# Optimization experiments

Hardware: AMD Instinct MI355X
Metric: run time of the kernel (lower is better)

Reference implementation:

```python
import jax, jax.numpy as jnp
import numpy as np

N, D, H, K = 32768, 1024, 8, 2048
HD = D // H
SIM_THRESH = 0.9


def setup_inputs() -> dict:
    key = jax.random.key(0)
    ks = jax.random.split(key, 12)
    s = 1.0 / np.sqrt(D)
    return {
        "roi_features": jax.random.normal(ks[0], (N, D), jnp.float32),
        "w_score": jax.random.uniform(ks[1], (1, D), jnp.float32, -s, s),
        "b_score": jax.random.uniform(ks[2], (1,), jnp.float32, -s, s),
        "wq": jax.random.uniform(ks[3], (D, D), jnp.float32, -s, s),
        "bq": jax.random.uniform(ks[4], (D,), jnp.float32, -s, s),
        "wk": jax.random.uniform(ks[5], (D, D), jnp.float32, -s, s),
        "bk": jax.random.uniform(ks[6], (D,), jnp.float32, -s, s),
        "wv": jax.random.uniform(ks[7], (D, D), jnp.float32, -s, s),
        "bv": jax.random.uniform(ks[8], (D,), jnp.float32, -s, s),
        "wo": jax.random.uniform(ks[9], (D, 2 * D), jnp.float32, -s, s),
        "bo": jax.random.uniform(ks[10], (D,), jnp.float32, -s, s),
    }


def _cross_frame_attention(src, dst, wq, bq, wk, bk, wv, bv, wo, bo):
    # src, dst: [K, D] -> fused dst: [K, D]
    q = (dst @ wq.T + bq).reshape(-1, H, HD).transpose(1, 0, 2)  # [H,K,HD]
    k = (src @ wk.T + bk).reshape(-1, H, HD).transpose(1, 0, 2)
    v = (src @ wv.T + bv).reshape(-1, H, HD).transpose(1, 0, 2)
    logits = jnp.einsum("hqd,hkd->hqk", q, k) / np.sqrt(HD)
    qn = q / (jnp.linalg.norm(q, axis=-1, keepdims=True) + 1e-6)
    kn = k / (jnp.linalg.norm(k, axis=-1, keepdims=True) + 1e-6)
    sim = jnp.einsum("hqd,hkd->hqk", qn, kn)
    valid = sim > SIM_THRESH
    logits = jnp.where(valid, logits, -10000.0)
    attn = jax.nn.softmax(logits, axis=-1)
    has_match = jnp.any(valid, axis=-1, keepdims=True)
    attn = jnp.where(has_match, attn, 0.0)  # dropout is identity in eval
    agg = jnp.einsum("hqk,hkd->hqd", attn, v).transpose(1, 0, 2).reshape(dst.shape[0], D)
    return jnp.concatenate([agg, dst], axis=-1) @ wo.T + bo


def reference(roi_features, w_score, b_score, wq, bq, wk, bk, wv, bv, wo, bo):
    # _global_fusion_fallback path (no temporal context set)
    scores = (roi_features @ w_score.T + b_score)[:, 0]  # [N]
    _, topk_idx = jax.lax.top_k(scores, K)
    selected = roi_features[topk_idx]  # [K, D]
    fused = _cross_frame_attention(selected, selected, wq, bq, wk, bk, wv, bv, wo, bo)
    return roi_features.at[topk_idx].set(0.5 * selected + 0.5 * fused)
```

## Files before the change

### kernel.cpp

```cpp
#include <hip/hip_runtime.h>
#include <cstddef>

typedef unsigned int u32;
typedef unsigned short u16;
typedef short v8s __attribute__((ext_vector_type(8)));
typedef float v4f __attribute__((ext_vector_type(4)));

#define N_ROWS 32768
#define DIM 1024
#define NHEAD 8
#define HD 128
#define KSEL 2048

static __device__ __forceinline__ u16 f2bf(float f) {
  u32 u = __float_as_uint(f);
  u32 r = (u + 0x7FFFu + ((u >> 16) & 1u)) >> 16;
  return (u16)r;
}
static __device__ __forceinline__ float bf2f(u16 b) {
  return __uint_as_float(((u32)b) << 16);
}
static __device__ __forceinline__ u32 mono(float s) {
  u32 b = __float_as_uint(s);
  return (b & 0x80000000u) ? ~b : (b | 0x80000000u);
}

__global__ __launch_bounds__(256) void score_copy_kernel(
    const float* __restrict__ roi, const float* __restrict__ wsc,
    const float* __restrict__ bsc, float* __restrict__ out,
    float* __restrict__ scores) {
  const int w = threadIdx.x >> 6, lane = threadIdx.x & 63;
  const int row = blockIdx.x * 4 + w;
  const float4* r4 = (const float4*)(roi + (size_t)row * DIM);
  const float4* w4 = (const float4*)wsc;
  float4* o4 = (float4*)(out + (size_t)row * DIM);
  float sum = 0.f;
#pragma unroll
  for (int rep = 0; rep < 4; ++rep) {
    int i = rep * 64 + lane;
    float4 v = r4[i];
    float4 q = w4[i];
    sum += v.x * q.x + v.y * q.y + v.z * q.z + v.w * q.w;
    o4[i] = v;
  }
#pragma unroll
  for (int d = 1; d < 64; d <<= 1) sum += __shfl_xor(sum, d);
  if (lane == 0) scores[row] = sum + bsc[0];
}

__global__ __launch_bounds__(256) void cvt4_kernel(
    const float* __restrict__ wq, const float* __restrict__ wk,
    const float* __restrict__ wv, const float* __restrict__ wo,
    u16* __restrict__ wqb, u16* __restrict__ wkb,
    u16* __restrict__ wvb, u16* __restrict__ wob) {
  const int M = DIM * DIM;
  long long i = ((long long)blockIdx.x * 256 + threadIdx.x) * 4;
  const float* src;
  u16* dst;
  if (i < M) {
    src = wq; dst = wqb;
  } else if (i < 2LL * M) {
    src = wk; dst = wkb; i -= M;
  } else if (i < 3LL * M) {
    src = wv; dst = wvb; i -= 2LL * M;
  } else {
    src = wo; dst = wob; i -= 3LL * M;
  }
  float4 v = *(const float4*)(src + i);
  ushort4 o = make_ushort4(f2bf(v.x), f2bf(v.y), f2bf(v.z), f2bf(v.w));
  *(ushort4*)(dst + i) = o;
}

__global__ __launch_bounds__(1024) void topk_kernel(const float* __restrict__ scores,
                                                    int* __restrict__ out_idx) {
  __shared__ u32 hist[256];
  __shared__ int sneed;
  __shared__ u32 sprefix;
  __shared__ int scan_gt[1024];
  __shared__ int scan_eq[1024];
  const int tid = threadIdx.x;
  if (tid == 0) { sneed = KSEL; sprefix = 0u; }
  for (int pass = 0; pass < 4; ++pass) {
    const int shift = 24 - pass * 8;
    if (tid < 256) hist[tid] = 0u;
    __syncthreads();
    const u32 prefmask = (pass == 0) ? 0u : (0xFFFFFFFFu << (shift + 8));
    const u32 pref = sprefix;
    for (int i = tid; i < N_ROWS; i += 1024) {
      u32 key = mono(scores[i]);
      if ((key & prefmask) == pref) atomicAdd(&hist[(key >> shift) & 255u], 1u);
    }
    __syncthreads();
    if (tid == 0) {
      int need = sneed;
      u32 cum = 0;
      int b = 255;
      for (; b > 0; --b) {
        if (cum + hist[b] >= (u32)need) break;
        cum += hist[b];
      }
      sneed = need - (int)cum;
      sprefix = pref | ((u32)b << shift);
    }
    __syncthreads();
  }
  const u32 T = sprefix;
  const int base = tid * 32;
  int cgt = 0, ceq = 0;
  for (int j = 0; j < 32; ++j) {
    u32 key = mono(scores[base + j]);
    cgt += (key > T);
    ceq += (key == T);
  }
  scan_gt[tid] = cgt;
  scan_eq[tid] = ceq;
  __syncthreads();
  for (int off = 1; off < 1024; off <<= 1) {
    int a = (tid >= off) ? scan_gt[tid - off] : 0;
    int b = (tid >= off) ? scan_eq[tid - off] : 0;
    __syncthreads();
    scan_gt[tid] += a;
    scan_eq[tid] += b;
    __syncthreads();
  }
  const int gt_off = scan_gt[tid] - cgt;
  const int eq_off = scan_eq[tid] - ceq;
  const int total_gt = scan_gt[1023];
  int g = gt_off, e = eq_off;
  for (int j = 0; j < 32; ++j) {
    u32 key = mono(scores[base + j]);
    if (key > T) {
      out_idx[g++] = base + j;
    } else if (key == T) {
      if (total_gt + e < KSEL) out_idx[total_gt + e] = base + j;
      e++;
    }
  }
}

__global__ __launch_bounds__(256) void gather_kernel(const float* __restrict__ out,
                                                     const int* __restrict__ idx,
                                                     u16* __restrict__ xo) {
  const int j = blockIdx.x;
  const int row = idx[j];
  const int c = threadIdx.x * 4;
  float4 v = *(const float4*)(out + (size_t)row * DIM + c);
  ushort4 o = make_ushort4(f2bf(v.x), f2bf(v.y), f2bf(v.z), f2bf(v.w));
  *(ushort4*)(xo + (size_t)j * 2048 + 1024 + c) = o;
}

template <int OUT_MODE>
__global__ __launch_bounds__(256) void gemm_xwt_kernel(
    const u16* __restrict__ A, int lda, const u16* __restrict__ W, int ldw,
    const float* __restrict__ bias, void* __restrict__ Cout, int ldc, int Kd) {
  __shared__ __align__(16) u16 As[64][40];
  __shared__ __align__(16) u16 Bs[64][40];
  const int m0 = blockIdx.y * 64, n0 = blockIdx.x * 64;
  const int w = threadIdx.x >> 6, lane = threadIdx.x & 63;
  const int t = lane & 15, quad = lane >> 4;
  const int srow = threadIdx.x >> 2, skc = (threadIdx.x & 3) * 8;
  v4f acc[4];
#pragma unroll
  for (int i = 0; i < 4; ++i) acc[i] = (v4f){0.f, 0.f, 0.f, 0.f};
  const u16* aptr = A + (size_t)(m0 + srow) * lda + skc;
  const u16* bptr = W + (size_t)(n0 + srow) * ldw + skc;
  uint4 areg = *(const uint4*)aptr;
  uint4 breg = *(const uint4*)bptr;
  for (int k0 = 0; k0 < Kd; k0 += 32) {
    __syncthreads();
    *(uint4*)&As[srow][skc] = areg;
    *(uint4*)&Bs[srow][skc] = breg;
    __syncthreads();
    const int kn = (k0 + 32 < Kd) ? k0 + 32 : 0;
    areg = *(const uint4*)(aptr + kn);
    breg = *(const uint4*)(bptr + kn);
    v8s af = *(const v8s*)&As[w * 16 + t][quad * 8];
#pragma unroll
    for (int nc = 0; nc < 4; ++nc) {
      v8s bf = *(const v8s*)&Bs[nc * 16 + t][quad * 8];
      acc[nc] = __builtin_amdgcn_mfma_f32_16x16x32_bf16(af, bf, acc[nc], 0, 0, 0);
    }
  }
#pragma unroll
  for (int nc = 0; nc < 4; ++nc) {
    const int col = n0 + nc * 16 + t;
    const float bv = bias[col];
    if (OUT_MODE == 2) {
      const int h = col >> 7, hd = col & 127;
      const int row0 = m0 + w * 16 + quad * 4;
      ushort4 pk = make_ushort4(f2bf(acc[nc][0] + bv), f2bf(acc[nc][1] + bv),
                                f2bf(acc[nc][2] + bv), f2bf(acc[nc][3] + bv));
      *(ushort4*)((u16*)Cout + (size_t)h * (HD * KSEL) + (size_t)hd * KSEL + row0) = pk;
    } else {
#pragma unroll
      for (int r = 0; r < 4; ++r) {
        const int row = m0 + w * 16 + quad * 4 + r;
        float v = acc[nc][r] + bv;
        if (OUT_MODE == 1)
          ((float*)Cout)[(size_t)row * ldc + col] = v;
        else
          ((u16*)Cout)[(size_t)row * ldc + col] = f2bf(v);
      }
    }
  }
}

__global__ __launch_bounds__(256) void norms_kernel(const u16* __restrict__ qb,
                                                    const u16* __restrict__ kb,
                                                    float* __restrict__ rnq,
                                                    float* __restrict__ rnk) {
  const int w = threadIdx.x >> 6, lane = threadIdx.x & 63;
  int p = blockIdx.x * 4 + w;
  const u16* src;
  float* dst;
  if (p < NHEAD * KSEL) {
    src = qb;
    dst = rnq;
  } else {
    src = kb;
    dst = rnk;
    p -= NHEAD * KSEL;
  }
  const int h = p >> 11, m = p & 2047;
  u32 u = *(const u32*)&src[(size_t)m * DIM + h * HD + lane * 2];
  float a = bf2f((u16)(u & 0xffffu)), b = bf2f((u16)(u >> 16));
  float ss = a * a + b * b;
#pragma unroll
  for (int d = 1; d < 64; d <<= 1) ss += __shfl_xor(ss, d);
  if (lane == 0) dst[h * KSEL + m] = 1.0f / (sqrtf(ss) + 1e-6f);
}

__global__ __launch_bounds__(256) void attn_kernel(
    const u16* __restrict__ qb, const u16* __restrict__ kb, const u16* __restrict__ vt,
    const float* __restrict__ rnq, const float* __restrict__ rnk,
    u16* __restrict__ xo) {
  const int h = blockIdx.x >> 5;
  const int q0 = (blockIdx.x & 31) * 64;
  const int tid = threadIdx.x;
  const int w = tid >> 6, lane = tid & 63;
  const int t = lane & 15, quad = lane >> 4;
  const int m0 = q0 + w * 16;

  __shared__ __align__(16) u16 Ks[32][136];
  __shared__ __align__(16) u16 Vs[128][40];
  __shared__ __align__(16) u16 Ps[4][16][40];
  __shared__ float rks[32];

  v8s qf[4];
#pragma unroll
  for (int c = 0; c < 4; ++c)
    qf[c] = *(const v8s*)&qb[(size_t)(m0 + t) * DIM + h * HD + c * 32 + quad * 8];
  float rq[4];
#pragma unroll
  for (int r = 0; r < 4; ++r) rq[r] = rnq[h * KSEL + m0 + quad * 4 + r];

  float li[4] = {0.f, 0.f, 0.f, 0.f};
  v4f o[8];
#pragma unroll
  for (int f = 0; f < 8; ++f) o[f] = (v4f){0.f, 0.f, 0.f, 0.f};

  const float scale = 0.08838834764831845f;

  const int kkey = tid >> 4;
  const int khc = (tid & 15) * 8;
  const int vhd = tid >> 2;
  const int vch = (tid & 3) * 8;
  const u16* kbase = kb + (size_t)h * HD + khc;
  const u16* vbase = vt + (size_t)h * (HD * KSEL) + (size_t)vhd * KSEL + vch;
  const float* rkb = rnk + h * KSEL + tid;

  uint4 kreg0, kreg1, vreg0, vreg1;
  float rkreg = 0.f;
#define PREFETCH(KT)                                                   \
  do {                                                                 \
    kreg0 = *(const uint4*)(kbase + (size_t)((KT) + kkey) * DIM);      \
    kreg1 = *(const uint4*)(kbase + (size_t)((KT) + kkey + 16) * DIM); \
    vreg0 = *(const uint4*)(vbase + (KT));                             \
    vreg1 = *(const uint4*)(vbase + (size_t)64 * KSEL + (KT));         \
    if (tid < 32) rkreg = rkb[(KT)];                                   \
  } while (0)

  PREFETCH(0);
  for (int kt = 0; kt < KSEL; kt += 32) {
    __syncthreads();
    *(uint4*)&Ks[kkey][khc] = kreg0;
    *(uint4*)&Ks[kkey + 16][khc] = kreg1;
    *(uint4*)&Vs[vhd][vch] = vreg0;
    *(uint4*)&Vs[vhd + 64][vch] = vreg1;
    if (tid < 32) rks[tid] = rkreg;
    __syncthreads();
    const int ktn = (kt + 32 < KSEL) ? kt + 32 : 0;
    PREFETCH(ktn);

    v4f s0 = (v4f){0.f, 0.f, 0.f, 0.f}, s1 = (v4f){0.f, 0.f, 0.f, 0.f};
#pragma unroll
    for (int c = 0; c < 4; ++c) {
      v8s k0f = *(const v8s*)&Ks[t][c * 32 + quad * 8];
      v8s k1f = *(const v8s*)&Ks[16 + t][c * 32 + quad * 8];
      s0 = __builtin_amdgcn_mfma_f32_16x16x32_bf16(qf[c], k0f, s0, 0, 0, 0);
      s1 = __builtin_amdgcn_mfma_f32_16x16x32_bf16(qf[c], k1f, s1, 0, 0, 0);
    }
    const float rk0 = rks[t], rk1 = rks[16 + t];
#pragma unroll
    for (int r = 0; r < 4; ++r) {
      const float S0 = s0[r], S1 = s1[r];
      const float p0 = (S0 * rq[r] * rk0 > 0.9f) ? __expf(S0 * scale) : 0.f;
      const float p1 = (S1 * rq[r] * rk1 > 0.9f) ? __expf(S1 * scale) : 0.f;
      li[r] += p0 + p1;
      Ps[w][quad * 4 + r][t] = f2bf(p0);
      Ps[w][quad * 4 + r][16 + t] = f2bf(p1);
    }
    v8s pf = *(const v8s*)&Ps[w][t][quad * 8];
#pragma unroll
    for (int f = 0; f < 8; ++f) {
      v8s vf = *(const v8s*)&Vs[f * 16 + t][quad * 8];
      o[f] = __builtin_amdgcn_mfma_f32_16x16x32_bf16(pf, vf, o[f], 0, 0, 0);
    }
  }
#undef PREFETCH
  float inv[4];
#pragma unroll
  for (int r = 0; r < 4; ++r) {
    float l = li[r];
    l += __shfl_xor(l, 1);
    l += __shfl_xor(l, 2);
    l += __shfl_xor(l, 4);
    l += __shfl_xor(l, 8);
    inv[r] = (l > 0.f) ? 1.0f / l : 0.f;
  }
#pragma unroll
  for (int f = 0; f < 8; ++f)
#pragma unroll
    for (int r = 0; r < 4; ++r)
      xo[(size_t)(m0 + quad * 4 + r) * 2048 + h * HD + f * 16 + t] = f2bf(o[f][r] * inv[r]);
}

__global__ __launch_bounds__(256) void final_kernel(float* __restrict__ out,
                                                    const int* __restrict__ idx,
                                                    const float* __restrict__ fused) {
  const int j = blockIdx.x;
  const int row = idx[j];
  const int c = threadIdx.x * 4;
  float4 a = *(const float4*)(out + (size_t)row * DIM + c);
  float4 f = *(const float4*)(fused + (size_t)j * DIM + c);
  float4 rv;
  rv.x = 0.5f * (a.x + f.x);
  rv.y = 0.5f * (a.y + f.y);
  rv.z = 0.5f * (a.z + f.z);
  rv.w = 0.5f * (a.w + f.w);
  *(float4*)(out + (size_t)row * DIM + c) = rv;
}

extern "C" void kernel_launch(void* const* d_in, const int* in_sizes, int n_in,
                              void* d_out, int out_size, void* d_ws, size_t ws_size,
                              hipStream_t stream) {
  const float* roi = (const float*)d_in[0];
  const float* w_score = (const float*)d_in[1];
  const float* b_score = (const float*)d_in[2];
  const float* wq = (const float*)d_in[3];
  const float* bq = (const float*)d_in[4];
  const float* wk = (const float*)d_in[5];
  const float* bk = (const float*)d_in[6];
  const float* wv = (const float*)d_in[7];
  const float* bv = (const float*)d_in[8];
  const float* wo = (const float*)d_in[9];
  const float* bo = (const float*)d_in[10];
  float* out = (float*)d_out;

  char* p = (char*)d_ws;
  auto alloc = [&](size_t bytes) {
    char* r = p;
    p += (bytes + 255) & ~(size_t)255;
    return r;
  };
  float* scores = (float*)alloc((size_t)N_ROWS * 4);
  int* topk = (int*)alloc((size_t)KSEL * 4);
  u16* wqb = (u16*)alloc((size_t)DIM * DIM * 2);
  u16* wkb = (u16*)alloc((size_t)DIM * DIM * 2);
  u16* wvb = (u16*)alloc((size_t)DIM * DIM * 2);
  u16* wob = (u16*)alloc((size_t)DIM * 2 * DIM * 2);
  u16* xo = (u16*)alloc((size_t)KSEL * 2048 * 2);
  u16* qbuf = (u16*)alloc((size_t)KSEL * DIM * 2);
  u16* kbuf = (u16*)alloc((size_t)KSEL * DIM * 2);
  u16* vtbuf = (u16*)alloc((size_t)KSEL * DIM * 2);
  float* rnq = (float*)alloc((size_t)NHEAD * KSEL * 4);
  float* rnk = (float*)alloc((size_t)NHEAD * KSEL * 4);
  float* fused = (float*)alloc((size_t)KSEL * DIM * 4);

  score_copy_kernel<<<N_ROWS / 4, 256, 0, stream>>>(roi, w_score, b_score, out, scores);
  cvt4_kernel<<<5 * DIM * DIM / 1024, 256, 0, stream>>>(wq, wk, wv, wo, wqb, wkb, wvb, wob);
  topk_kernel<<<1, 1024, 0, stream>>>(scores, topk);
  gather_kernel<<<KSEL, 256, 0, stream>>>(out, topk, xo);
  gemm_xwt_kernel<0><<<dim3(16, 32), 256, 0, stream>>>(xo + 1024, 2048, wqb, DIM, bq, qbuf, DIM, DIM);
  gemm_xwt_kernel<0><<<dim3(16, 32), 256, 0, stream>>>(xo + 1024, 2048, wkb, DIM, bk, kbuf, DIM, DIM);
  gemm_xwt_kernel<2><<<dim3(16, 32), 256, 0, stream>>>(xo + 1024, 2048, wvb, DIM, bv, vtbuf, DIM, DIM);
  norms_kernel<<<2 * NHEAD * KSEL / 4, 256, 0, stream>>>(qbuf, kbuf, rnq, rnk);
  attn_kernel<<<NHEAD * 32, 256, 0, stream>>>(qbuf, kbuf, vtbuf, rnq, rnk, xo);
  gemm_xwt_kernel<1><<<dim3(16, 32), 256, 0, stream>>>(xo, 2048, wob, 2048, bo, fused, DIM, 2048);
  final_kernel<<<KSEL, 256, 0, stream>>>(out, topk, fused);
}
```

Measured before the change: 496.2 us.

## Rewrite top-k radix select with register-cached keys and 3 parallel passes

The top-k selection kernel now loads each thread's 32 scores once into registers as monotone keys instead of re-reading global memory in every pass. It uses three 11/11/10-bit radix passes over a 2048-bin histogram instead of four 8-bit passes. The serial single-thread bucket search is replaced with a parallel suffix scan over the histogram. This targets the latency of a single-block kernel that sits on the critical path, at the cost of more shared memory, more registers and a longer scan per pass.

```diff
diff --git a/kernel.cpp b/kernel.cpp
--- a/kernel.cpp
+++ b/kernel.cpp
@@ -73,44 +73,71 @@
 
 __global__ __launch_bounds__(1024) void topk_kernel(const float* __restrict__ scores,
                                                     int* __restrict__ out_idx) {
-  __shared__ u32 hist[256];
+  __shared__ u32 hist[2048];
   __shared__ int sneed;
-  __shared__ u32 sprefix;
+  __shared__ u32 sbucket;
   __shared__ int scan_gt[1024];
   __shared__ int scan_eq[1024];
   const int tid = threadIdx.x;
-  if (tid == 0) { sneed = KSEL; sprefix = 0u; }
-  for (int pass = 0; pass < 4; ++pass) {
-    const int shift = 24 - pass * 8;
-    if (tid < 256) hist[tid] = 0u;
-    __syncthreads();
-    const u32 prefmask = (pass == 0) ? 0u : (0xFFFFFFFFu << (shift + 8));
-    const u32 pref = sprefix;
-    for (int i = tid; i < N_ROWS; i += 1024) {
-      u32 key = mono(scores[i]);
-      if ((key & prefmask) == pref) atomicAdd(&hist[(key >> shift) & 255u], 1u);
-    }
-    __syncthreads();
-    if (tid == 0) {
-      int need = sneed;
-      u32 cum = 0;
-      int b = 255;
-      for (; b > 0; --b) {
-        if (cum + hist[b] >= (u32)need) break;
-        cum += hist[b];
+
+  u32 keys[32];
+  const float4* sp = (const float4*)(scores + (size_t)tid * 32);
+#pragma unroll
+  for (int j = 0; j < 8; ++j) {
+    float4 v = sp[j];
+    keys[j * 4 + 0] = mono(v.x);
+    keys[j * 4 + 1] = mono(v.y);
+    keys[j * 4 + 2] = mono(v.z);
+    keys[j * 4 + 3] = mono(v.w);
+  }
+  if (tid == 0) sneed = KSEL;
+
+  u32 pref = 0;
+  const int shifts[3] = {21, 10, 0};
+#pragma unroll
+  for (int pass = 0; pass < 3; ++pass) {
+    const int shift = shifts[pass];
+    hist[tid] = 0u;
+    hist[tid + 1024] = 0u;
+    __syncthreads();
+    const u32 prefmask = (pass == 0) ? 0u : (0xFFFFFFFFu << shifts[pass - 1]);
+#pragma unroll
+    for (int j = 0; j < 32; ++j) {
+      u32 k = keys[j];
+      if ((k & prefmask) == pref) atomicAdd(&hist[(k >> shift) & 2047u], 1u);
+    }
+    __syncthreads();
+    for (int off = 1; off < 2048; off <<= 1) {
+      u32 v0 = (tid + off < 2048) ? hist[tid + off] : 0u;
+      u32 v1 = (tid + 1024 + off < 2048) ? hist[tid + 1024 + off] : 0u;
+      __syncthreads();
+      hist[tid] += v0;
+      hist[tid + 1024] += v1;
+      __syncthreads();
+    }
+    const int need = sneed;
+    __syncthreads();
+#pragma unroll
+    for (int e = 0; e < 2; ++e) {
+      const int i = tid + e * 1024;
+      const int s = (int)hist[i];
+      const int snx = (i < 2047) ? (int)hist[i + 1] : 0;
+      if (s >= need && snx < need) {
+        sbucket = (u32)i;
+        sneed = need - snx;
       }
-      sneed = need - (int)cum;
-      sprefix = pref | ((u32)b << shift);
-    }
-    __syncthreads();
-  }
-  const u32 T = sprefix;
+    }
+    __syncthreads();
+    pref |= (sbucket << shift);
+  }
+  const u32 T = pref;
+
   const int base = tid * 32;
   int cgt = 0, ceq = 0;
+#pragma unroll
   for (int j = 0; j < 32; ++j) {
-    u32 key = mono(scores[base + j]);
-    cgt += (key > T);
-    ceq += (key == T);
+    cgt += (keys[j] > T);
+    ceq += (keys[j] == T);
   }
   scan_gt[tid] = cgt;
   scan_eq[tid] = ceq;
@@ -127,8 +154,9 @@
   const int eq_off = scan_eq[tid] - ceq;
   const int total_gt = scan_gt[1023];
   int g = gt_off, e = eq_off;
+#pragma unroll
   for (int j = 0; j < 32; ++j) {
-    u32 key = mono(scores[base + j]);
+    u32 key = keys[j];
     if (key > T) {
       out_idx[g++] = base + j;
     } else if (key == T) {
```

Measured after the change: 436.5 us. 12.0% less time.
